# Optimization experiments

Hardware: AMD Instinct MI355X
Metric: run time of the kernel (lower is better)

## Reference

```python
import jax, jax.numpy as jnp
import numpy as np

B, S, E, H = 4, 2048, 1024, 16
D = E // H  # head_dim = 64


def setup_inputs() -> dict:
    key = jax.random.key(0)
    ks = jax.random.split(key, 10)
    scale = 1.0 / np.sqrt(E)
    return {
        "decoder_sequence": jax.random.normal(ks[0], (B, S, E), dtype=jnp.float32),
        # stacked per-head projection weights (math-equivalent to per-head nn.Linear)
        "Wq": jax.random.normal(ks[1], (H, E, D), dtype=jnp.float32) * scale,
        "bq": jnp.zeros((H, D), dtype=jnp.float32),
        "Wk": jax.random.normal(ks[2], (H, E, D), dtype=jnp.float32) * scale,
        "bk": jnp.zeros((H, D), dtype=jnp.float32),
        "Wv": jax.random.normal(ks[3], (H, E, D), dtype=jnp.float32) * scale,
        "bv": jnp.zeros((H, D), dtype=jnp.float32),
        "Wo": jax.random.normal(ks[4], (E, E), dtype=jnp.float32) * scale,
        "bo": jnp.zeros((E,), dtype=jnp.float32),
    }


def reference(decoder_sequence, Wq, bq, Wk, bk, Wv, bv, Wo, bo):
    x = decoder_sequence  # [B,S,E]
    # per-head Q/K/V projections, batched over the head axis
    Q = jnp.einsum('bse,hed->bhsd', x, Wq) + bq[:, None, :]
    K = jnp.einsum('bse,hed->bhsd', x, Wk) + bk[:, None, :]
    V = jnp.einsum('bse,hed->bhsd', x, Wv) + bv[:, None, :]
    # scaled scores with causal mask (upper triangle -> -inf)
    A = jnp.einsum('bhid,bhjd->bhij', Q, K) / jnp.sqrt(jnp.float32(D))
    causal = jnp.tril(jnp.ones((S, S), dtype=bool))  # True where allowed
    A = jnp.where(causal, A, -jnp.inf)
    A = jax.nn.softmax(A, axis=-1)
    Hout = jnp.einsum('bhij,bhjd->bhid', A, V)  # [B,H,S,D]
    # concat heads: [B,S,H*D]
    concat = jnp.transpose(Hout, (0, 2, 1, 3)).reshape(B, S, H * D)
    return concat @ Wo.T + bo
```

## Files before the change

### kernel.cpp

```cpp
#include <hip/hip_runtime.h>
#include <stdint.h>
#include <stddef.h>

typedef __bf16 bf16;
typedef __bf16 bf16x8 __attribute__((ext_vector_type(8)));
typedef __bf16 bf16x4 __attribute__((ext_vector_type(4)));
typedef float  f32x4  __attribute__((ext_vector_type(4)));
typedef float  f32x16 __attribute__((ext_vector_type(16)));
typedef unsigned short ush;
typedef ush ush8 __attribute__((ext_vector_type(8)));
typedef unsigned int uint;

#define B_  4
#define S_  2048
#define E_  1024
#define H_  16
#define D_  64
#define M_  (B_*S_)
#define K_  E_
#define QSCALE 0.18033688011112042f
#define SSHIFT 16.0f

__device__ __forceinline__ void gload_lds16(const void* g, void* l) {
  __builtin_amdgcn_global_load_lds((const __attribute__((address_space(1))) void*)g,
                                   (__attribute__((address_space(3))) void*)l, 16, 0, 0);
}
__device__ __forceinline__ f32x4 mfma16(bf16x8 a, bf16x8 b, f32x4 c) {
  return __builtin_amdgcn_mfma_f32_16x16x32_bf16(a, b, c, 0, 0, 0);
}
__device__ __forceinline__ f32x16 mfma32(bf16x8 a, bf16x8 b, f32x16 c) {
  return __builtin_amdgcn_mfma_f32_32x32x16_bf16(a, b, c, 0, 0, 0);
}
__device__ __forceinline__ int swz4(int row, int ch) { return ch ^ ((row >> 1) & 3); }
__device__ __forceinline__ uint cvtpk(float lo, float hi) {
  uint r;
  asm("v_cvt_pk_bf16_f32 %0, %1, %2" : "=v"(r) : "v"(lo), "v"(hi));
  return r;
}

__global__ void prep_kernel(const float* __restrict__ x, bf16* __restrict__ Xbf,
                            const float* __restrict__ Wo, bf16* __restrict__ Wot,
                            const float* __restrict__ Wq, const float* __restrict__ Wk,
                            const float* __restrict__ Wv, bf16* __restrict__ Wp) {
  __shared__ float t[64][65];
  const int tid = threadIdx.x;
  if (blockIdx.x < 2048) {
    const int n4x = (M_ * K_) / 4, n4w = (E_ * E_) / 4;
    int idx = blockIdx.x * 256 + tid;
    const int stride = 2048 * 256;
    for (int i = idx; i < n4x + n4w; i += stride) {
      const float4 v = (i < n4x) ? ((const float4*)x)[i] : ((const float4*)Wo)[i - n4x];
      union { bf16 b[4]; ushort4 u; } cv;
      cv.b[0] = (bf16)v.x; cv.b[1] = (bf16)v.y; cv.b[2] = (bf16)v.z; cv.b[3] = (bf16)v.w;
      if (i < n4x) ((ushort4*)Xbf)[i] = cv.u;
      else         ((ushort4*)Wot)[i - n4x] = cv.u;
    }
  } else {
    const int pb = blockIdx.x - 2048;
    const int wh = pb >> 4;
    const int which = wh >> 4, h = wh & 15;
    const int e0 = (pb & 15) << 6;
    const float* src = (which == 0) ? Wq : (which == 1 ? Wk : Wv);
    src += (size_t)h * (E_ * D_);
    #pragma unroll
    for (int i = 0; i < 4; ++i) {
      int fi = tid + 256 * i;
      int e = fi >> 4, c = fi & 15;
      float4 v = *(const float4*)(src + (size_t)(e0 + e) * D_ + c * 4);
      t[c * 4 + 0][e] = v.x; t[c * 4 + 1][e] = v.y;
      t[c * 4 + 2][e] = v.z; t[c * 4 + 3][e] = v.w;
    }
    __syncthreads();
    #pragma unroll
    for (int i = 0; i < 2; ++i) {
      int cid = tid + 256 * i;
      int d = cid >> 3, cc = cid & 7;
      ush8 o;
      #pragma unroll
      for (int j = 0; j < 8; ++j) {
        union { bf16 b; ush u; } cv; cv.b = (bf16)t[d][cc * 8 + j]; o[j] = cv.u;
      }
      *(ush8*)(Wp + ((size_t)which * 1024 + h * 64 + d) * K_ + e0 + cc * 8) = o;
    }
  }
}

template <int MODE>
__launch_bounds__(256, 3)
__global__ void gemm_kernel(const bf16* __restrict__ A, const bf16* __restrict__ Bm,
                            int Ntot,
                            const float* __restrict__ bias0, const float* __restrict__ bias1,
                            const float* __restrict__ bias2,
                            bf16* __restrict__ Qo, bf16* __restrict__ Ko, bf16* __restrict__ Vto,
                            float* __restrict__ Fo) {
  __shared__ __align__(16) bf16 lds_a[2][128 * 32];
  __shared__ __align__(16) bf16 lds_b[2][128 * 32];
  const int tid = threadIdx.x;
  const int lane = tid & 63;
  const int w = tid >> 6;
  const int wr = w >> 1, wc = w & 1;
  int mt, nt;
  if (MODE == 0) {
    const int xcd = blockIdx.x & 7;
    const int idx = blockIdx.x >> 3;
    mt = ((xcd >> 1) << 4) + (idx & 15);
    nt = (xcd & 1) * 12 + (idx >> 4);
  } else {
    const int nblk = Ntot >> 7;
    const int qch = gridDim.x >> 3;
    const int swz = (blockIdx.x & 7) * qch + (blockIdx.x >> 3);
    mt = swz / nblk; nt = swz % nblk;
  }
  const int m0 = mt << 7, n0 = nt << 7;

  f32x4 acc[4][4] = {};

  auto stage = [&](int buf, int kt) {
    #pragma unroll
    for (int i = 0; i < 2; ++i) {
      int cb = (w * 2 + i) * 64;
      int cid = cb + lane;
      int row = cid >> 2, cir = cid & 3;
      int lch = swz4(row, cir);
      const bf16* ga = A  + (size_t)(m0 + row) * K_ + kt * 32 + lch * 8;
      const bf16* gb = Bm + (size_t)(n0 + row) * K_ + kt * 32 + lch * 8;
      gload_lds16(ga, &lds_a[buf][cb * 8]);
      gload_lds16(gb, &lds_b[buf][cb * 8]);
    }
  };

  const int NT = K_ / 32;
  stage(0, 0);
  for (int kt = 0; kt < NT; ++kt) {
    if (kt + 1 < NT) {
      stage((kt + 1) & 1, kt + 1);
      asm volatile("s_waitcnt vmcnt(4)" ::: "memory");
    } else {
      asm volatile("s_waitcnt vmcnt(0)" ::: "memory");
    }
    __builtin_amdgcn_s_barrier();
    __builtin_amdgcn_sched_barrier(0);
    const bf16x8* pa = (const bf16x8*)&lds_a[kt & 1][0];
    const bf16x8* pb = (const bf16x8*)&lds_b[kt & 1][0];
    bf16x8 af[4], bfr[4];
    #pragma unroll
    for (int mb = 0; mb < 4; ++mb) {
      int row = wr * 64 + mb * 16 + (lane & 15);
      af[mb] = pa[row * 4 + swz4(row, lane >> 4)];
    }
    #pragma unroll
    for (int nb = 0; nb < 4; ++nb) {
      int row = wc * 64 + nb * 16 + (lane & 15);
      bfr[nb] = pb[row * 4 + swz4(row, lane >> 4)];
    }
    __builtin_amdgcn_s_setprio(1);
    #pragma unroll
    for (int mb = 0; mb < 4; ++mb)
      #pragma unroll
      for (int nb = 0; nb < 4; ++nb)
        acc[mb][nb] = mfma16(af[mb], bfr[nb], acc[mb][nb]);
    __builtin_amdgcn_s_setprio(0);
    asm volatile("s_waitcnt lgkmcnt(0)" ::: "memory");
    __builtin_amdgcn_s_barrier();
  }

  #pragma unroll
  for (int mb = 0; mb < 4; ++mb) {
    #pragma unroll
    for (int nb = 0; nb < 4; ++nb) {
      const int ni  = n0 + wc * 64 + nb * 16 + (lane & 15);
      const int mi0 = m0 + wr * 64 + mb * 16 + (lane >> 4) * 4;
      if (MODE == 0) {
        const int which = ni >> 10;
        const int col = ni & 1023;
        const float* bp = (which == 0) ? bias0 : (which == 1 ? bias1 : bias2);
        const float bv = bp[col];
        const int hh = col >> 6, d = col & 63;
        const int b = mi0 >> 11, s0r = mi0 & 2047;
        if (which == 2) {
          bf16x4 st;
          #pragma unroll
          for (int r = 0; r < 4; ++r) st[r] = (bf16)(acc[mb][nb][r] + bv);
          *(bf16x4*)(Vto + ((size_t)((b * H_ + hh) * D_ + d)) * S_ + s0r) = st;
        } else {
          bf16* dst = (which == 0) ? Qo : Ko;
          const float sc = (which == 0) ? QSCALE : 1.f;
          #pragma unroll
          for (int r = 0; r < 4; ++r)
            dst[(((size_t)(b * H_ + hh)) * S_ + (s0r + r)) * D_ + d] =
                (bf16)((acc[mb][nb][r] + bv) * sc);
        }
      } else {
        #pragma unroll
        for (int r = 0; r < 4; ++r)
          Fo[(size_t)(mi0 + r) * E_ + ni] = acc[mb][nb][r] + bias0[ni];
      }
    }
  }
}

struct QTile {
  bf16x8 qf[4];
  f32x16 oacc[2];
  float l;
};
struct KVF {
  bf16x8 k0[4], k1[4];
  bf16x8 v0[4], v1[4];
};

__device__ __forceinline__ void init_q(QTile& S, const bf16* qrow, int hi) {
  #pragma unroll
  for (int kc = 0; kc < 4; ++kc)
    S.qf[kc] = *(const bf16x8*)(qrow + (2 * kc + hi) * 8);
  #pragma unroll
  for (int r = 0; r < 16; ++r) { S.oacc[0][r] = 0.f; S.oacc[1][r] = 0.f; }
  S.l = 0.f;
}

__device__ __forceinline__ void load_frags(KVF& F, const bf16* klds, const bf16* vlds,
                                           int sub, int hi, int ln) {
  const bf16* kbase = klds + sub * (64 * 64);
  const int lxor = (ln & 7) ^ ((ln >> 3) & 3);
  #pragma unroll
  for (int kc = 0; kc < 4; ++kc) {
    int ch = (2 * kc + hi) ^ lxor;
    F.k0[kc] = *(const bf16x8*)&kbase[ln * 64 + ch * 8];
    F.k1[kc] = *(const bf16x8*)&kbase[(32 + ln) * 64 + ch * 8];
  }
  #pragma unroll
  for (int ks = 0; ks < 4; ++ks) {
    int cf = sub * 8 + 2 * ks + hi;
    int ch = cf ^ (ln & 15);
    F.v0[ks] = *(const bf16x8*)&vlds[ln * 128 + ch * 8];
    F.v1[ks] = *(const bf16x8*)&vlds[(32 + ln) * 128 + ch * 8];
  }
}

__device__ __forceinline__ void step_one(QTile& S, const KVF& F,
                                         int kv0, int qb_, int qg_, int hi) {
  if (kv0 > qb_ + 31) return;
  f32x16 s0 = {}, s1 = {};
  __builtin_amdgcn_s_setprio(1);
  #pragma unroll
  for (int kc = 0; kc < 4; ++kc) {
    s0 = mfma32(F.k0[kc], S.qf[kc], s0);
    s1 = mfma32(F.k1[kc], S.qf[kc], s1);
  }
  __builtin_amdgcn_s_setprio(0);
  if (kv0 + 63 > qb_) {
    #pragma unroll
    for (int r = 0; r < 16; ++r) {
      int crow = (r & 3) + 8 * (r >> 2) + 4 * hi;
      if (kv0 + crow > qg_)      s0[r] = -1e30f;
      if (kv0 + 32 + crow > qg_) s1[r] = -1e30f;
    }
  }
  #pragma unroll
  for (int r = 0; r < 16; ++r) {
    s0[r] = exp2f(s0[r] - SSHIFT);
    s1[r] = exp2f(s1[r] - SSHIFT);
  }
  bf16x8 pf[4];
  #pragma unroll
  for (int mtl = 0; mtl < 2; ++mtl) {
    #pragma unroll
    for (int c = 0; c < 2; ++c) {
      const f32x16& p = mtl ? s1 : s0;
      uint wa = cvtpk(p[8 * c + 0], p[8 * c + 1]);
      uint wb = cvtpk(p[8 * c + 2], p[8 * c + 3]);
      uint wcx = cvtpk(p[8 * c + 4], p[8 * c + 5]);
      uint wd = cvtpk(p[8 * c + 6], p[8 * c + 7]);
      asm("v_permlane32_swap_b32 %0, %1" : "+v"(wa), "+v"(wcx));
      asm("v_permlane32_swap_b32 %0, %1" : "+v"(wb), "+v"(wd));
      union { uint u[4]; bf16x8 v; } cvt;
      cvt.u[0] = wa; cvt.u[1] = wb; cvt.u[2] = wcx; cvt.u[3] = wd;
      pf[mtl * 2 + c] = cvt.v;
    }
  }
  const bf16 one_ = (bf16)1.f;
  const bf16x8 vones = {one_, one_, one_, one_, one_, one_, one_, one_};
  f32x16 lt = {};
  __builtin_amdgcn_s_setprio(1);
  #pragma unroll
  for (int ks = 0; ks < 4; ++ks) lt = mfma32(vones, pf[ks], lt);
  #pragma unroll
  for (int ks = 0; ks < 4; ++ks) {
    S.oacc[0] = mfma32(F.v0[ks], pf[ks], S.oacc[0]);
    S.oacc[1] = mfma32(F.v1[ks], pf[ks], S.oacc[1]);
  }
  __builtin_amdgcn_s_setprio(0);
  S.l += lt[0];
}

__device__ __forceinline__ void store_o(const QTile& S, bf16* orow, int hi) {
  float rinv = 1.f / S.l;
  #pragma unroll
  for (int dm = 0; dm < 2; ++dm) {
    #pragma unroll
    for (int g = 0; g < 4; ++g) {
      bf16x4 st;
      #pragma unroll
      for (int i = 0; i < 4; ++i) st[i] = (bf16)(S.oacc[dm][4 * g + i] * rinv);
      *(bf16x4*)(orow + dm * 32 + g * 8 + hi * 4) = st;
    }
  }
}

__launch_bounds__(256, 2)
__global__ void attn_kernel(const bf16* __restrict__ Q, const bf16* __restrict__ K,
                            const bf16* __restrict__ Vt, bf16* __restrict__ Cc) {
  __shared__ __align__(16) bf16 k_lds[2][128 * 64];
  __shared__ __align__(16) bf16 v_lds[2][64 * 128];
  const int tid = threadIdx.x, lane = tid & 63, w = tid >> 6;
  const int hi = lane >> 5, ln = lane & 31;
  const int bid = blockIdx.x;
  const int bh = bid & 63;
  const int x = bid >> 6;
  const bf16* Kb = K  + (size_t)bh * (S_ * D_);
  const bf16* Vb = Vt + (size_t)bh * (D_ * S_);
  const int b = bh >> 4, hh = bh & 15;

  const int qbA = x * 128 + w * 32,        qgA = qbA + ln;
  const int qbB = (15 - x) * 128 + w * 32, qgB = qbB + ln;
  const int nphA = x + 1, nphB = 16 - x;

  QTile SA, SB;
  init_q(SA, Q + ((size_t)bh * S_ + qgA) * D_, hi);
  init_q(SB, Q + ((size_t)bh * S_ + qgB) * D_, hi);

  auto stage2 = [&](int buf, int ph) {
    const int kv0 = ph << 7;
    #pragma unroll
    for (int i = 0; i < 4; ++i) {
      int cb = (w * 4 + i) * 64;
      int cid = cb + lane;
      int row = cid >> 3, cir = cid & 7;
      int lch = cir ^ (row & 7) ^ ((row >> 3) & 3);
      gload_lds16(Kb + (size_t)(kv0 + row) * D_ + lch * 8, &k_lds[buf][cb * 8]);
      int rowv = cid >> 4, cirv = cid & 15;
      int lchv = cirv ^ (rowv & 15);
      gload_lds16(Vb + (size_t)rowv * S_ + kv0 + lchv * 8, &v_lds[buf][cb * 8]);
    }
  };

  stage2(0, 0);
  __syncthreads();
  for (int ph = 0; ph < nphB; ++ph) {
    const int cur = ph & 1;
    if (ph + 1 < nphB) stage2(cur ^ 1, ph + 1);
    const int kv0 = ph << 7;
    {
      KVF F0;
      load_frags(F0, k_lds[cur], v_lds[cur], 0, hi, ln);
      if (ph < nphA) step_one(SA, F0, kv0, qbA, qgA, hi);
      step_one(SB, F0, kv0, qbB, qgB, hi);
    }
    {
      KVF F1;
      load_frags(F1, k_lds[cur], v_lds[cur], 1, hi, ln);
      if (ph < nphA) step_one(SA, F1, kv0 + 64, qbA, qgA, hi);
      step_one(SB, F1, kv0 + 64, qbB, qgB, hi);
    }
    __syncthreads();
  }

  store_o(SA, Cc + ((size_t)(b * S_ + qgA)) * E_ + hh * D_, hi);
  store_o(SB, Cc + ((size_t)(b * S_ + qgB)) * E_ + hh * D_, hi);
}

extern "C" void kernel_launch(void* const* d_in, const int* in_sizes, int n_in,
                              void* d_out, int out_size, void* d_ws, size_t ws_size,
                              hipStream_t stream) {
  const float* x  = (const float*)d_in[0];
  const float* Wq = (const float*)d_in[1];
  const float* bq = (const float*)d_in[2];
  const float* Wk = (const float*)d_in[3];
  const float* bk = (const float*)d_in[4];
  const float* Wv = (const float*)d_in[5];
  const float* bv = (const float*)d_in[6];
  const float* Wo = (const float*)d_in[7];
  const float* bo = (const float*)d_in[8];
  float* out = (float*)d_out;

  uint8_t* ws = (uint8_t*)d_ws;
  bf16* Xbf   = (bf16*)(ws + 0);
  bf16* Wpack = (bf16*)(ws + 16777216);
  bf16* Wot   = (bf16*)(ws + 23068672);
  bf16* Qb    = (bf16*)(ws + 25165824);
  bf16* Kb    = (bf16*)(ws + 41943040);
  bf16* Vtb   = (bf16*)(ws + 75497472);
  bf16* Cc    = Xbf;

  prep_kernel<<<dim3(2816), 256, 0, stream>>>(x, Xbf, Wo, Wot, Wq, Wk, Wv, Wpack);

  gemm_kernel<0><<<dim3(64 * 24), 256, 0, stream>>>(Xbf, Wpack, 3072, bq, bk, bv,
                                                    Qb, Kb, Vtb, nullptr);

  attn_kernel<<<dim3(512), 256, 0, stream>>>(Qb, Kb, Vtb, Cc);

  gemm_kernel<1><<<dim3(64 * 8), 256, 0, stream>>>(Cc, Wot, 1024, bo, nullptr, nullptr,
                                                   nullptr, nullptr, nullptr, out);
}
```

Baseline: 176.1 us.

## Split paired causal Q tiles into separate blocks with 64-wide KV staging

The attention kernel no longer pairs a short and a long causal query tile in one block to balance work. Each block now handles one 128-row query tile, streaming 64-row K/V tiles through a smaller double-buffered LDS, with twice as many blocks and launch bounds raised to four blocks per CU. The aim is more occupancy and finer scheduling granularity. In exchange, per-block work is uneven and the longest blocks are launched first, K/V reuse per LDS load drops, and there are more barriers per unit of work.

Measured after the change: 253.2 us. 43.8% more time.

```diff
diff --git a/kernel.cpp b/kernel.cpp
--- a/kernel.cpp
+++ b/kernel.cpp
@@ -219,21 +219,19 @@
 }
 
 __device__ __forceinline__ void load_frags(KVF& F, const bf16* klds, const bf16* vlds,
-                                           int sub, int hi, int ln) {
-  const bf16* kbase = klds + sub * (64 * 64);
+                                           int hi, int ln) {
   const int lxor = (ln & 7) ^ ((ln >> 3) & 3);
   #pragma unroll
   for (int kc = 0; kc < 4; ++kc) {
     int ch = (2 * kc + hi) ^ lxor;
-    F.k0[kc] = *(const bf16x8*)&kbase[ln * 64 + ch * 8];
-    F.k1[kc] = *(const bf16x8*)&kbase[(32 + ln) * 64 + ch * 8];
+    F.k0[kc] = *(const bf16x8*)&klds[ln * 64 + ch * 8];
+    F.k1[kc] = *(const bf16x8*)&klds[(32 + ln) * 64 + ch * 8];
   }
   #pragma unroll
   for (int ks = 0; ks < 4; ++ks) {
-    int cf = sub * 8 + 2 * ks + hi;
-    int ch = cf ^ (ln & 15);
-    F.v0[ks] = *(const bf16x8*)&vlds[ln * 128 + ch * 8];
-    F.v1[ks] = *(const bf16x8*)&vlds[(32 + ln) * 128 + ch * 8];
+    int ch = (2 * ks + hi) ^ lxor;
+    F.v0[ks] = *(const bf16x8*)&vlds[ln * 64 + ch * 8];
+    F.v1[ks] = *(const bf16x8*)&vlds[(32 + ln) * 64 + ch * 8];
   }
 }
 
@@ -307,66 +305,51 @@
   }
 }
 
-__launch_bounds__(256, 2)
+__launch_bounds__(256, 4)
 __global__ void attn_kernel(const bf16* __restrict__ Q, const bf16* __restrict__ K,
                             const bf16* __restrict__ Vt, bf16* __restrict__ Cc) {
-  __shared__ __align__(16) bf16 k_lds[2][128 * 64];
-  __shared__ __align__(16) bf16 v_lds[2][64 * 128];
+  __shared__ __align__(16) bf16 k_lds[2][64 * 64];
+  __shared__ __align__(16) bf16 v_lds[2][64 * 64];
   const int tid = threadIdx.x, lane = tid & 63, w = tid >> 6;
   const int hi = lane >> 5, ln = lane & 31;
   const int bid = blockIdx.x;
   const int bh = bid & 63;
-  const int x = bid >> 6;
+  const int j = 15 - (bid >> 6);
   const bf16* Kb = K  + (size_t)bh * (S_ * D_);
   const bf16* Vb = Vt + (size_t)bh * (D_ * S_);
   const int b = bh >> 4, hh = bh & 15;
 
-  const int qbA = x * 128 + w * 32,        qgA = qbA + ln;
-  const int qbB = (15 - x) * 128 + w * 32, qgB = qbB + ln;
-  const int nphA = x + 1, nphB = 16 - x;
-
-  QTile SA, SB;
-  init_q(SA, Q + ((size_t)bh * S_ + qgA) * D_, hi);
-  init_q(SB, Q + ((size_t)bh * S_ + qgB) * D_, hi);
-
-  auto stage2 = [&](int buf, int ph) {
-    const int kv0 = ph << 7;
-    #pragma unroll
-    for (int i = 0; i < 4; ++i) {
-      int cb = (w * 4 + i) * 64;
+  const int qb = j * 128 + w * 32, qg = qb + ln;
+  const int nt = 2 * j + 2;
+
+  QTile S;
+  init_q(S, Q + ((size_t)bh * S_ + qg) * D_, hi);
+
+  auto stage64 = [&](int buf, int t) {
+    const int kv0 = t << 6;
+    #pragma unroll
+    for (int i = 0; i < 2; ++i) {
+      int cb = (w * 2 + i) * 64;
       int cid = cb + lane;
       int row = cid >> 3, cir = cid & 7;
       int lch = cir ^ (row & 7) ^ ((row >> 3) & 3);
       gload_lds16(Kb + (size_t)(kv0 + row) * D_ + lch * 8, &k_lds[buf][cb * 8]);
-      int rowv = cid >> 4, cirv = cid & 15;
-      int lchv = cirv ^ (rowv & 15);
-      gload_lds16(Vb + (size_t)rowv * S_ + kv0 + lchv * 8, &v_lds[buf][cb * 8]);
+      gload_lds16(Vb + (size_t)row * S_ + kv0 + lch * 8, &v_lds[buf][cb * 8]);
     }
   };
 
-  stage2(0, 0);
+  stage64(0, 0);
   __syncthreads();
-  for (int ph = 0; ph < nphB; ++ph) {
-    const int cur = ph & 1;
-    if (ph + 1 < nphB) stage2(cur ^ 1, ph + 1);
-    const int kv0 = ph << 7;
-    {
-      KVF F0;
-      load_frags(F0, k_lds[cur], v_lds[cur], 0, hi, ln);
-      if (ph < nphA) step_one(SA, F0, kv0, qbA, qgA, hi);
-      step_one(SB, F0, kv0, qbB, qgB, hi);
-    }
-    {
-      KVF F1;
-      load_frags(F1, k_lds[cur], v_lds[cur], 1, hi, ln);
-      if (ph < nphA) step_one(SA, F1, kv0 + 64, qbA, qgA, hi);
-      step_one(SB, F1, kv0 + 64, qbB, qgB, hi);
-    }
+  for (int t = 0; t < nt; ++t) {
+    const int cur = t & 1;
+    if (t + 1 < nt) stage64(cur ^ 1, t + 1);
+    KVF F;
+    load_frags(F, k_lds[cur], v_lds[cur], hi, ln);
+    step_one(S, F, t * 64, qb, qg, hi);
     __syncthreads();
   }
 
-  store_o(SA, Cc + ((size_t)(b * S_ + qgA)) * E_ + hh * D_, hi);
-  store_o(SB, Cc + ((size_t)(b * S_ + qgB)) * E_ + hh * D_, hi);
+  store_o(S, Cc + ((size_t)(b * S_ + qg)) * E_ + hh * D_, hi);
 }
 
 extern "C" void kernel_launch(void* const* d_in, const int* in_sizes, int n_in,
@@ -397,7 +380,7 @@
   gemm_kernel<0><<<dim3(64 * 24), 256, 0, stream>>>(Xbf, Wpack, 3072, bq, bk, bv,
                                                     Qb, Kb, Vtb, nullptr);
 
-  attn_kernel<<<dim3(512), 256, 0, stream>>>(Qb, Kb, Vtb, Cc);
+  attn_kernel<<<dim3(1024), 256, 0, stream>>>(Qb, Kb, Vtb, Cc);
 
   gemm_kernel<1><<<dim3(64 * 8), 256, 0, stream>>>(Cc, Wot, 1024, bo, nullptr, nullptr,
                                                    nullptr, nullptr, nullptr, out);
```
